# Kernel optimization log

Hardware: AMD Instinct MI355X
Metric: run time of the kernel (lower is better)

The kernel has to match this reference:

```python
import jax, jax.numpy as jnp
import numpy as np

B, N, P, K = 128, 256, 256, 4  # batches, obs points, pred points, nfunc


def setup_inputs() -> dict:
    key = jax.random.key(0)
    k1, k2, k3, k4, k5 = jax.random.split(key, 5)
    # squared distances: symmetric obs-obs block with zero diagonal + obs-pred block
    d_oo = jax.random.uniform(k1, (B, N, N), dtype=jnp.float32) * 25.0
    d_oo = 0.5 * (d_oo + jnp.swapaxes(d_oo, -1, -2))
    d_oo = d_oo * (1.0 - jnp.eye(N, dtype=jnp.float32))
    d_op = jax.random.uniform(k2, (B, N, P), dtype=jnp.float32) * 25.0
    C = jnp.concatenate([d_oo, d_op], axis=-1)  # (B, N, N+P)
    val = jax.random.normal(k3, (B, N, K), dtype=jnp.float32)
    bad = jax.random.randint(k4, (B, N), 0, 10) == 0
    rm = jax.random.normal(k5, (K, 1), dtype=jnp.float32) * 0.1  # MyKF.rm param
    eps_param = -1.5 * jnp.ones((K,), dtype=jnp.float32)          # DistOA.eps param
    return {"C": C, "val": val, "rm": rm, "eps_param": eps_param, "bad": bad}


def _forward(C, val, rm, eps_param, bad):
    n = C.shape[-2]
    # MyKF: x = d2 * sigmoid(rm)/rmax^2 (rmax=1); kernel (1+x)exp(-x)  -> (K,B,n,n+p)
    rmk = jax.nn.sigmoid(rm)[..., None, None]            # (K,1,1,1)
    x = rmk * C[None]
    Cf = (1.0 + x) * jnp.exp(-x)                          # (K,B,n,n+p)
    b = Cf[..., n:]                                       # (K,B,n,p)
    Cm = Cf[..., :n]                                      # (K,B,n,n)
    # implicit: add sigmoid(eps) on the diagonal
    eps = jax.nn.sigmoid(eps_param)[:, None, None, None]  # (K,1,1,1)
    Cm = Cm + eps * jnp.eye(n, dtype=C.dtype)
    # NaN/bad masking: zero bad rows of b; zero xor(bad_i, bad_j) entries of C
    good = (~bad).astype(C.dtype)                         # (B,n)
    b = b * good[None, :, :, None]
    keep = (~(bad[:, :, None] ^ bad[:, None, :])).astype(C.dtype)  # (B,n,n)
    Cm = Cm * keep[None]
    # batched solve + clamp-based reweighting (edging=False)
    d = jnp.linalg.solve(Cm, b)                           # (K,B,n,p)
    wg = jnp.clip((jnp.abs(d).sum(-2, keepdims=True) - 1.0) * 2.0, 0.0, 1.0)
    d1 = b / Cm.sum(-1, keepdims=True)
    r = d * (1.0 - wg) + d1 * (wg / jnp.clip(d1.sum(-2, keepdims=True), 1.0, None))
    # neddvalgrad=False -> val detached before nan_to_num
    val0 = jnp.nan_to_num(jax.lax.stop_gradient(val))     # (B,n,K)
    return jnp.einsum('kbjp,bjk->bpk', r, val0)           # (B,p,K)


def reference(C, val, rm, eps_param, bad):
    return _forward(C, val, rm, eps_param, bad)
```

## Files before the change

### kernel.cpp

```cpp
#include <hip/hip_runtime.h>
#include <cstddef>

#define NN 256
#define PP 256
#define BB 128
#define KK 4
#define NSYS 512
#define PW 32
#define NPAN (NN/PW)

__device__ __forceinline__ float sigmoidf_(float x){ return 1.0f/(1.0f+expf(-x)); }

__global__ __launch_bounds__(256) void build_kernel(
    const float* __restrict__ C, const float* __restrict__ rm,
    const float* __restrict__ epsp, const int* __restrict__ bad,
    float* __restrict__ A, float* __restrict__ rowsum, int s0)
{
  const int si = blockIdx.x;
  const int ls = si >> 8;
  const int i  = si & 255;
  const int s  = s0 + ls;
  const int k  = s >> 7;
  const int b  = s & 127;
  const int j  = threadIdx.x;

  const float sk = sigmoidf_(rm[k]);
  const float ek = sigmoidf_(epsp[k]);
  const bool bad_i = bad[b*NN + i] != 0;
  const bool bad_j = bad[b*NN + j] != 0;

  float c  = C[((size_t)b*NN + i)*(NN+PP) + j];
  float x  = sk * c;
  float cf = (1.0f + x) * expf(-x);
  if (i == j) cf += ek;
  float keep = (bad_i == bad_j) ? 1.0f : 0.0f;
  float a = cf * keep;
  A[((size_t)ls*NN + i)*NN + j] = a;

  __shared__ float red[256];
  red[j] = a; __syncthreads();
  #pragma unroll
  for (int off = 128; off > 0; off >>= 1){
    if (j < off) red[j] += red[j + off];
    __syncthreads();
  }
  if (j == 0) rowsum[ls*NN + i] = red[0];
}

__global__ __launch_bounds__(512, 4) void lu_kernel(
    float* __restrict__ Aall, int* __restrict__ permAll)
{
  __shared__ float panel[NN][PW+1];
  __shared__ float linv[PW][PW+1];
  __shared__ float uinv[PW][PW+1];
  __shared__ float urow[PW][NN-PW];
  __shared__ float redv[2][8];
  __shared__ int   redi[2][8];
  __shared__ int   pivseq[NN];
  __shared__ int   actlist[NN];
  __shared__ unsigned char pickedsh[NN];
  __shared__ int   nact;

  const int ls = blockIdx.x;
  float* __restrict__ A = Aall + (size_t)ls*NN*NN;
  const int t = threadIdx.x;
  const int lane = t & 63, wid = t >> 6;
  bool picked = false;
  if (t < NN) pickedsh[t] = 0;

  for (int I = 0; I < NPAN; ++I){
    const int col0 = I*PW;
    const int W = NN - col0 - PW;
    if (t == 0) nact = 0;
    __syncthreads();

    for (int e = t; e < NN*PW; e += 512){
      int r = e >> 5, c = e & 31;
      panel[r][c] = A[(size_t)r*NN + col0 + c];
    }
    __syncthreads();

    {
      float v = -1.0f; int vi = 0;
      if (t < NN && !picked){ v = fabsf(panel[t][0]); vi = t; }
      #pragma unroll
      for (int off = 32; off > 0; off >>= 1){
        float ov = __shfl_down(v, off); int oi = __shfl_down(vi, off);
        if (ov > v){ v = ov; vi = oi; }
      }
      if (lane == 0){ redv[0][wid] = v; redi[0][wid] = vi; }
    }
    __syncthreads();

    for (int c = 0; c < PW; ++c){
      const int par = c & 1;
      float bv = redv[par][0]; int p = redi[par][0];
      #pragma unroll
      for (int w = 1; w < 8; ++w)
        if (redv[par][w] > bv){ bv = redv[par][w]; p = redi[par][w]; }
      if (t == p){ picked = true; pickedsh[t] = 1; pivseq[col0+c] = t; }

      float nv = -1.0f; int ni = t;
      if (t < NN && !picked){
        const float rdia = 1.0f / panel[p][c];
        float m = panel[t][c] * rdia;
        panel[t][c] = m;
        float nxt = -1.0f;
        #pragma unroll
        for (int j = 0; j < PW; ++j){
          if (j > c){
            float u = panel[t][j] - m * panel[p][j];
            panel[t][j] = u;
            if (j == c+1) nxt = fabsf(u);
          }
        }
        nv = nxt;
      }
      #pragma unroll
      for (int off = 32; off > 0; off >>= 1){
        float ov = __shfl_down(nv, off); int oi = __shfl_down(ni, off);
        if (ov > nv){ nv = ov; ni = oi; }
      }
      if (lane == 0){ redv[par^1][wid] = nv; redi[par^1][wid] = ni; }
      __syncthreads();
    }

    if (t >= 256){
      const int jj = t - 256;
      if (jj < W){
        const int j = col0 + PW + jj;
        float u[PW];
        #pragma unroll
        for (int c = 0; c < PW; ++c) u[c] = A[(size_t)pivseq[col0+c]*NN + j];
        #pragma unroll
        for (int c = 0; c < PW; ++c){
          const int pc = pivseq[col0+c];
          float sv = u[c];
          #pragma unroll
          for (int k2 = 0; k2 < PW; ++k2)
            if (k2 < c) sv -= panel[pc][k2] * u[k2];
          u[c] = sv;
          urow[c][jj] = sv;
          A[(size_t)pc*NN + j] = sv;
        }
      }
    } else if (t < PW){
      const int cth = t;
      for (int r = cth; r < PW; ++r){
        float sv = (r == cth) ? 1.0f : 0.0f;
        const int pr = pivseq[col0+r];
        for (int k2 = cth; k2 < r; ++k2) sv -= panel[pr][k2] * linv[k2][cth];
        linv[r][cth] = sv;
      }
    } else if (t >= 64 && t < 64+PW){
      const int cth = t - 64;
      for (int r = cth; r >= 0; --r){
        float sv = (r == cth) ? 1.0f : 0.0f;
        const int pr = pivseq[col0+r];
        for (int k2 = r+1; k2 <= cth; ++k2) sv -= panel[pr][k2] * uinv[k2][cth];
        uinv[r][cth] = sv / panel[pr][r];
      }
    } else if (t >= 128 && t < 192){
      #pragma unroll
      for (int q = 0; q < 4; ++q){
        int r = (t-128)*4 + q;
        if (!pickedsh[r]){ int pos = atomicAdd(&nact, 1); actlist[pos] = r; }
      }
    }
    __syncthreads();

    for (int e = t; e < PW*PW; e += 512){
      int r = e >> 5, c2 = e & 31;
      A[(size_t)pivseq[col0+r]*NN + col0 + c2] = (r > c2) ? linv[r][c2] : uinv[r][c2];
    }
    for (int e = t; e < NN*PW; e += 512){
      int r = e >> 5, c2 = e & 31;
      if (!pickedsh[r]) A[(size_t)r*NN + col0 + c2] = panel[r][c2];
    }

    if (W > 0){
      for (int i0 = wid*2; i0 < W; i0 += 16){
        const int r0 = actlist[i0];
        const int r1 = actlist[i0+1];
        float4* R0 = (float4*)(A + (size_t)r0*NN + col0 + PW);
        float4* R1 = (float4*)(A + (size_t)r1*NN + col0 + PW);
        if (lane*4 < W){
          float4 a0 = R0[lane];
          float4 a1 = R1[lane];
          #pragma unroll
          for (int c = 0; c < PW; ++c){
            float4 u4 = *(const float4*)&urow[c][lane*4];
            float p0 = panel[r0][c], p1 = panel[r1][c];
            a0.x -= p0*u4.x; a0.y -= p0*u4.y; a0.z -= p0*u4.z; a0.w -= p0*u4.w;
            a1.x -= p1*u4.x; a1.y -= p1*u4.y; a1.z -= p1*u4.z; a1.w -= p1*u4.w;
          }
          R0[lane] = a0;
          R1[lane] = a1;
        }
      }
    }
  }
  __syncthreads();
  if (t < NN) permAll[ls*NN + t] = pivseq[t];
}

__global__ __launch_bounds__(512, 2) void solve_epi_kernel(
    const float* __restrict__ Aall, const int* __restrict__ permAll,
    const float* __restrict__ rowsum,
    const float* __restrict__ C, const float* __restrict__ val,
    const int* __restrict__ bad, const float* __restrict__ rm,
    float* __restrict__ out, int s0)
{
  __shared__ float tile[NN][128];
  __shared__ float dblk[PW][PW+1];
  __shared__ __align__(16) float ubuf[4096];
  __shared__ int   perm[NN];

  int ls, c0;
  {
    const int g = blockIdx.x;
    if ((gridDim.x & 15) == 0){
      const int xcd = g & 7, idx = g >> 3;
      ls = xcd + 8*(idx >> 1);
      c0 = (idx & 1) * 128;
    } else {
      ls = g >> 1;
      c0 = (g & 1) * 128;
    }
  }
  const int s  = s0 + ls;
  const int k  = s >> 7, b = s & 127;
  const float* __restrict__ A = Aall + (size_t)ls*NN*NN;
  const float* __restrict__ rs = rowsum + ls*NN;
  const int t = threadIdx.x;
  const int lane = t & 63, wid = t >> 6;
  const int lane2 = lane + 64;
  const float sk = sigmoidf_(rm[k]);
  const int slr = t >> 3;
  const int sq4 = (t & 7) << 2;

  if (t < NN) perm[t] = permAll[ls*NN + t];
  __syncthreads();

  for (int e = t; e < NN*128; e += 512){
    int i = e >> 7, c = e & 127;
    int pi = perm[i];
    float cb = C[((size_t)b*NN + pi)*(NN+PP) + NN + c0 + c];
    float xb = sk * cb;
    float bf = (1.0f + xb) * expf(-xb);
    if (bad[b*NN + pi]) bf = 0.0f;
    tile[i][c] = bf;
  }
  __syncthreads();

  for (int J = 0; J < NPAN; ++J){
    const int j0 = J*PW;
    for (int e = t; e < PW*PW; e += 512){
      int r = e >> 5, c = e & 31;
      dblk[r][c] = A[(size_t)perm[j0+r]*NN + j0 + c];
    }
    __syncthreads();
    const int r0 = wid*4;
    float ya0 = tile[j0+r0+0][lane],  yb0 = tile[j0+r0+0][lane2];
    float ya1 = tile[j0+r0+1][lane],  yb1 = tile[j0+r0+1][lane2];
    float ya2 = tile[j0+r0+2][lane],  yb2 = tile[j0+r0+2][lane2];
    float ya3 = tile[j0+r0+3][lane],  yb3 = tile[j0+r0+3][lane2];
    for (int kk = 0; kk < r0; ++kk){
      float xa = tile[j0+kk][lane], xb = tile[j0+kk][lane2];
      float d0 = dblk[r0+0][kk], d1 = dblk[r0+1][kk], d2 = dblk[r0+2][kk], d3 = dblk[r0+3][kk];
      ya0 += d0*xa; yb0 += d0*xb;
      ya1 += d1*xa; yb1 += d1*xb;
      ya2 += d2*xa; yb2 += d2*xb;
      ya3 += d3*xa; yb3 += d3*xb;
    }
    {
      float xa0 = tile[j0+r0][lane],  xa1 = tile[j0+r0+1][lane],  xa2 = tile[j0+r0+2][lane];
      float xb0 = tile[j0+r0][lane2], xb1 = tile[j0+r0+1][lane2], xb2 = tile[j0+r0+2][lane2];
      float e10 = dblk[r0+1][r0];
      float e20 = dblk[r0+2][r0], e21 = dblk[r0+2][r0+1];
      float e30 = dblk[r0+3][r0], e31 = dblk[r0+3][r0+1], e32 = dblk[r0+3][r0+2];
      ya1 += e10*xa0;                         yb1 += e10*xb0;
      ya2 += e20*xa0 + e21*xa1;               yb2 += e20*xb0 + e21*xb1;
      ya3 += e30*xa0 + e31*xa1 + e32*xa2;     yb3 += e30*xb0 + e31*xb1 + e32*xb2;
    }
    __syncthreads();
    tile[j0+r0+0][lane]=ya0; tile[j0+r0+0][lane2]=yb0;
    tile[j0+r0+1][lane]=ya1; tile[j0+r0+1][lane2]=yb1;
    tile[j0+r0+2][lane]=ya2; tile[j0+r0+2][lane2]=yb2;
    tile[j0+r0+3][lane]=ya3; tile[j0+r0+3][lane2]=yb3;
    __syncthreads();
    const int nbelow = NN - j0 - PW;
    if (nbelow > 0){
      float xa[PW], xb[PW];
      #pragma unroll
      for (int kk = 0; kk < PW; ++kk){ xa[kk] = tile[j0+kk][lane]; xb[kk] = tile[j0+kk][lane2]; }
      for (int cb2 = 0; cb2 < nbelow; cb2 += 64){
        const int rows_c = (nbelow - cb2 < 64) ? (nbelow - cb2) : 64;
        if (t < rows_c*8)
          *(float4*)&ubuf[(slr<<5) + sq4] =
            *(const float4*)(A + (size_t)perm[j0+PW+cb2+slr]*NN + j0 + sq4);
        __syncthreads();
        const int rpw = rows_c >> 3;
        for (int p2 = 0; p2 < rpw; p2 += 2){
          const int lr0 = wid*rpw + p2;
          const int ia = j0 + PW + cb2 + lr0, ib = ia + 1;
          const float* __restrict__ S0 = &ubuf[lr0<<5];
          const float* __restrict__ S1 = &ubuf[(lr0+1)<<5];
          float a0a = tile[ia][lane], a0b = tile[ia][lane2];
          float a1a = tile[ib][lane], a1b = tile[ib][lane2];
          #pragma unroll
          for (int q = 0; q < 8; ++q){
            float4 a4 = *(const float4*)(S0 + (q<<2));
            float4 b4 = *(const float4*)(S1 + (q<<2));
            a0a -= a4.x*xa[q*4+0] + a4.y*xa[q*4+1] + a4.z*xa[q*4+2] + a4.w*xa[q*4+3];
            a0b -= a4.x*xb[q*4+0] + a4.y*xb[q*4+1] + a4.z*xb[q*4+2] + a4.w*xb[q*4+3];
            a1a -= b4.x*xa[q*4+0] + b4.y*xa[q*4+1] + b4.z*xa[q*4+2] + b4.w*xa[q*4+3];
            a1b -= b4.x*xb[q*4+0] + b4.y*xb[q*4+1] + b4.z*xb[q*4+2] + b4.w*xb[q*4+3];
          }
          tile[ia][lane] = a0a; tile[ia][lane2] = a0b;
          tile[ib][lane] = a1a; tile[ib][lane2] = a1b;
        }
        __syncthreads();
      }
    }
  }

  for (int J = NPAN-1; J >= 0; --J){
    const int j0 = J*PW;
    for (int e = t; e < PW*PW; e += 512){
      int r = e >> 5, c = e & 31;
      dblk[r][c] = A[(size_t)perm[j0+r]*NN + j0 + c];
    }
    __syncthreads();
    const int r0 = wid*4;
    float ya0=0.f, ya1=0.f, ya2=0.f, ya3=0.f;
    float yb0=0.f, yb1=0.f, yb2=0.f, yb3=0.f;
    for (int kk = r0+4; kk < PW; ++kk){
      float xa = tile[j0+kk][lane], xb = tile[j0+kk][lane2];
      float d0 = dblk[r0+0][kk], d1 = dblk[r0+1][kk], d2 = dblk[r0+2][kk], d3 = dblk[r0+3][kk];
      ya0 += d0*xa; yb0 += d0*xb;
      ya1 += d1*xa; yb1 += d1*xb;
      ya2 += d2*xa; yb2 += d2*xb;
      ya3 += d3*xa; yb3 += d3*xb;
    }
    {
      float xa0 = tile[j0+r0][lane],  xa1 = tile[j0+r0+1][lane];
      float xa2 = tile[j0+r0+2][lane], xa3 = tile[j0+r0+3][lane];
      float xb0 = tile[j0+r0][lane2],  xb1 = tile[j0+r0+1][lane2];
      float xb2 = tile[j0+r0+2][lane2], xb3 = tile[j0+r0+3][lane2];
      float e00=dblk[r0][r0], e01=dblk[r0][r0+1], e02=dblk[r0][r0+2], e03=dblk[r0][r0+3];
      float e11=dblk[r0+1][r0+1], e12=dblk[r0+1][r0+2], e13=dblk[r0+1][r0+3];
      float e22=dblk[r0+2][r0+2], e23=dblk[r0+2][r0+3];
      float e33=dblk[r0+3][r0+3];
      ya0 += e00*xa0 + e01*xa1 + e02*xa2 + e03*xa3;  yb0 += e00*xb0 + e01*xb1 + e02*xb2 + e03*xb3;
      ya1 += e11*xa1 + e12*xa2 + e13*xa3;            yb1 += e11*xb1 + e12*xb2 + e13*xb3;
      ya2 += e22*xa2 + e23*xa3;                      yb2 += e22*xb2 + e23*xb3;
      ya3 += e33*xa3;                                yb3 += e33*xb3;
    }
    __syncthreads();
    tile[j0+r0+0][lane]=ya0; tile[j0+r0+0][lane2]=yb0;
    tile[j0+r0+1][lane]=ya1; tile[j0+r0+1][lane2]=yb1;
    tile[j0+r0+2][lane]=ya2; tile[j0+r0+2][lane2]=yb2;
    tile[j0+r0+3][lane]=ya3; tile[j0+r0+3][lane2]=yb3;
    __syncthreads();
    if (j0 > 0){
      float xa[PW], xb[PW];
      #pragma unroll
      for (int kk = 0; kk < PW; ++kk){ xa[kk] = tile[j0+kk][lane]; xb[kk] = tile[j0+kk][lane2]; }
      for (int cb2 = 0; cb2 < j0; cb2 += 64){
        const int rows_c = (j0 - cb2 < 64) ? (j0 - cb2) : 64;
        if (t < rows_c*8)
          *(float4*)&ubuf[(slr<<5) + sq4] =
            *(const float4*)(A + (size_t)perm[cb2+slr]*NN + j0 + sq4);
        __syncthreads();
        const int rpw = rows_c >> 3;
        for (int p2 = 0; p2 < rpw; p2 += 2){
          const int lr0 = wid*rpw + p2;
          const int ia = cb2 + lr0, ib = ia + 1;
          const float* __restrict__ S0 = &ubuf[lr0<<5];
          const float* __restrict__ S1 = &ubuf[(lr0+1)<<5];
          float a0a = tile[ia][lane], a0b = tile[ia][lane2];
          float a1a = tile[ib][lane], a1b = tile[ib][lane2];
          #pragma unroll
          for (int q = 0; q < 8; ++q){
            float4 a4 = *(const float4*)(S0 + (q<<2));
            float4 b4 = *(const float4*)(S1 + (q<<2));
            a0a -= a4.x*xa[q*4+0] + a4.y*xa[q*4+1] + a4.z*xa[q*4+2] + a4.w*xa[q*4+3];
            a0b -= a4.x*xb[q*4+0] + a4.y*xb[q*4+1] + a4.z*xb[q*4+2] + a4.w*xb[q*4+3];
            a1a -= b4.x*xa[q*4+0] + b4.y*xa[q*4+1] + b4.z*xa[q*4+2] + b4.w*xa[q*4+3];
            a1b -= b4.x*xb[q*4+0] + b4.y*xb[q*4+1] + b4.z*xb[q*4+2] + b4.w*xb[q*4+3];
          }
          tile[ia][lane] = a0a; tile[ia][lane2] = a0b;
          tile[ib][lane] = a1a; tile[ib][lane2] = a1b;
        }
        __syncthreads();
      }
    }
  }

  {
    float sdva=0.f, sabsa=0.f, s1va=0.f, s1a=0.f;
    float sdvb=0.f, sabsb=0.f, s1vb=0.f, s1b=0.f;
    const int pa = c0 + lane, pb = c0 + lane2;
    for (int j = wid*32; j < wid*32 + 32; ++j){
      float v = val[(b*NN + j)*KK + k];
      if (v != v) v = 0.0f;
      const float rsj = rs[j];
      const bool bj = bad[b*NN + j] != 0;
      float da = tile[j][lane];
      float cba = C[((size_t)b*NN + j)*(NN+PP) + NN + pa];
      float xba = sk*cba;
      float boa = (1.0f+xba)*expf(-xba);
      if (bj) boa = 0.0f;
      float d1a = boa / rsj;
      sdva += da*v; sabsa += fabsf(da); s1va += d1a*v; s1a += d1a;
      float db = tile[j][lane2];
      float cbb = C[((size_t)b*NN + j)*(NN+PP) + NN + pb];
      float xbb = sk*cbb;
      float bob = (1.0f+xbb)*expf(-xbb);
      if (bj) bob = 0.0f;
      float d1b = bob / rsj;
      sdvb += db*v; sabsb += fabsf(db); s1vb += d1b*v; s1b += d1b;
    }
    __syncthreads();
    ubuf[(0*8 + wid)*128 + lane] = sdva;  ubuf[(0*8 + wid)*128 + lane2] = sdvb;
    ubuf[(1*8 + wid)*128 + lane] = sabsa; ubuf[(1*8 + wid)*128 + lane2] = sabsb;
    ubuf[(2*8 + wid)*128 + lane] = s1va;  ubuf[(2*8 + wid)*128 + lane2] = s1vb;
    ubuf[(3*8 + wid)*128 + lane] = s1a;   ubuf[(3*8 + wid)*128 + lane2] = s1b;
  }
  __syncthreads();
  if (t < 128){
    float sdv=0.f, sabs=0.f, s1v=0.f, s1=0.f;
    #pragma unroll
    for (int w = 0; w < 8; ++w){
      sdv  += ubuf[(0*8 + w)*128 + t];
      sabs += ubuf[(1*8 + w)*128 + t];
      s1v  += ubuf[(2*8 + w)*128 + t];
      s1   += ubuf[(3*8 + w)*128 + t];
    }
    float wg    = fminf(fmaxf((sabs - 1.0f)*2.0f, 0.0f), 1.0f);
    float denom = fmaxf(s1, 1.0f);
    out[((size_t)b*PP + c0 + t)*KK + k] = (1.0f - wg)*sdv + (wg/denom)*s1v;
  }
}

extern "C" void kernel_launch(void* const* d_in, const int* in_sizes, int n_in,
                              void* d_out, int out_size, void* d_ws, size_t ws_size,
                              hipStream_t stream)
{
  (void)in_sizes; (void)n_in; (void)out_size;
  const float* C    = (const float*)d_in[0];
  const float* val  = (const float*)d_in[1];
  const float* rm   = (const float*)d_in[2];
  const float* epsp = (const float*)d_in[3];
  const int*   bad  = (const int*)d_in[4];
  float* out = (float*)d_out;

  const size_t per_sys = (size_t)NN*NN*4 + (size_t)NN*4 + (size_t)NN*4;
  int chunk = (int)(ws_size / per_sys);
  if (chunk < 1)    chunk = 1;
  if (chunk > NSYS) chunk = NSYS;

  float* ws     = (float*)d_ws;
  float* A      = ws;
  float* rowsum = A + (size_t)chunk*NN*NN;
  int*   perm   = (int*)(rowsum + (size_t)chunk*NN);

  for (int s0 = 0; s0 < NSYS; s0 += chunk){
    int cs = (NSYS - s0 < chunk) ? (NSYS - s0) : chunk;
    build_kernel<<<cs*NN, 256, 0, stream>>>(C, rm, epsp, bad, A, rowsum, s0);
    lu_kernel<<<cs, 512, 0, stream>>>(A, perm);
    solve_epi_kernel<<<cs*2, 512, 0, stream>>>(A, perm, rowsum, C, val, bad, rm, out, s0);
  }
}
```

Baseline: 1.529 ms.

## Split solve kernel into four 64-column blocks of 256 threads per system

The triangular-solve/epilogue kernel now assigns 64 right-hand-side columns per block with 256 threads, launching four blocks per system instead of two 512-thread blocks with 128 columns. This halves shared memory per block so more blocks can reside per CU and spreads work over more blocks. In exchange, each block reloads the same LU panels from global/L2 memory, doubling that traffic, and the panel update now processes one row per thread group per pass.

```diff
diff --git a/kernel.cpp b/kernel.cpp
--- a/kernel.cpp
+++ b/kernel.cpp
@@ -204,28 +204,28 @@
   if (t < NN) permAll[ls*NN + t] = pivseq[t];
 }
 
-__global__ __launch_bounds__(512, 2) void solve_epi_kernel(
+__global__ __launch_bounds__(256, 2) void solve_epi_kernel(
     const float* __restrict__ Aall, const int* __restrict__ permAll,
     const float* __restrict__ rowsum,
     const float* __restrict__ C, const float* __restrict__ val,
     const int* __restrict__ bad, const float* __restrict__ rm,
     float* __restrict__ out, int s0)
 {
-  __shared__ float tile[NN][128];
+  __shared__ float tile[NN][64];
   __shared__ float dblk[PW][PW+1];
-  __shared__ __align__(16) float ubuf[4096];
+  __shared__ __align__(16) float ubuf[2048];
   __shared__ int   perm[NN];
 
   int ls, c0;
   {
     const int g = blockIdx.x;
-    if ((gridDim.x & 15) == 0){
+    if ((gridDim.x & 31) == 0){
       const int xcd = g & 7, idx = g >> 3;
-      ls = xcd + 8*(idx >> 1);
-      c0 = (idx & 1) * 128;
+      ls = xcd + 8*(idx >> 2);
+      c0 = (idx & 3) * 64;
     } else {
-      ls = g >> 1;
-      c0 = (g & 1) * 128;
+      ls = g >> 2;
+      c0 = (g & 2 ? 128 : 0) + (g & 1)*64;
     }
   }
   const int s  = s0 + ls;
@@ -233,20 +233,19 @@
   const float* __restrict__ A = Aall + (size_t)ls*NN*NN;
   const float* __restrict__ rs = rowsum + ls*NN;
   const int t = threadIdx.x;
-  const int lane = t & 63, wid = t >> 6;
-  const int lane2 = lane + 64;
+  const int ca = t & 31;
+  const int cb = ca + 32;
+  const int rg = t >> 5;
   const float sk = sigmoidf_(rm[k]);
-  const int slr = t >> 3;
-  const int sq4 = (t & 7) << 2;
 
   if (t < NN) perm[t] = permAll[ls*NN + t];
   __syncthreads();
 
-  for (int e = t; e < NN*128; e += 512){
-    int i = e >> 7, c = e & 127;
+  for (int e = t; e < NN*64; e += 256){
+    int i = e >> 6, c = e & 63;
     int pi = perm[i];
-    float cb = C[((size_t)b*NN + pi)*(NN+PP) + NN + c0 + c];
-    float xb = sk * cb;
+    float cbv = C[((size_t)b*NN + pi)*(NN+PP) + NN + c0 + c];
+    float xb = sk * cbv;
     float bf = (1.0f + xb) * expf(-xb);
     if (bad[b*NN + pi]) bf = 0.0f;
     tile[i][c] = bf;
@@ -255,18 +254,18 @@
 
   for (int J = 0; J < NPAN; ++J){
     const int j0 = J*PW;
-    for (int e = t; e < PW*PW; e += 512){
+    for (int e = t; e < PW*PW; e += 256){
       int r = e >> 5, c = e & 31;
       dblk[r][c] = A[(size_t)perm[j0+r]*NN + j0 + c];
     }
     __syncthreads();
-    const int r0 = wid*4;
-    float ya0 = tile[j0+r0+0][lane],  yb0 = tile[j0+r0+0][lane2];
-    float ya1 = tile[j0+r0+1][lane],  yb1 = tile[j0+r0+1][lane2];
-    float ya2 = tile[j0+r0+2][lane],  yb2 = tile[j0+r0+2][lane2];
-    float ya3 = tile[j0+r0+3][lane],  yb3 = tile[j0+r0+3][lane2];
+    const int r0 = rg*4;
+    float ya0 = tile[j0+r0+0][ca],  yb0 = tile[j0+r0+0][cb];
+    float ya1 = tile[j0+r0+1][ca],  yb1 = tile[j0+r0+1][cb];
+    float ya2 = tile[j0+r0+2][ca],  yb2 = tile[j0+r0+2][cb];
+    float ya3 = tile[j0+r0+3][ca],  yb3 = tile[j0+r0+3][cb];
     for (int kk = 0; kk < r0; ++kk){
-      float xa = tile[j0+kk][lane], xb = tile[j0+kk][lane2];
+      float xa = tile[j0+kk][ca], xb = tile[j0+kk][cb];
       float d0 = dblk[r0+0][kk], d1 = dblk[r0+1][kk], d2 = dblk[r0+2][kk], d3 = dblk[r0+3][kk];
       ya0 += d0*xa; yb0 += d0*xb;
       ya1 += d1*xa; yb1 += d1*xb;
@@ -274,8 +273,8 @@
       ya3 += d3*xa; yb3 += d3*xb;
     }
     {
-      float xa0 = tile[j0+r0][lane],  xa1 = tile[j0+r0+1][lane],  xa2 = tile[j0+r0+2][lane];
-      float xb0 = tile[j0+r0][lane2], xb1 = tile[j0+r0+1][lane2], xb2 = tile[j0+r0+2][lane2];
+      float xa0 = tile[j0+r0][ca],  xa1 = tile[j0+r0+1][ca],  xa2 = tile[j0+r0+2][ca];
+      float xb0 = tile[j0+r0][cb],  xb1 = tile[j0+r0+1][cb],  xb2 = tile[j0+r0+2][cb];
       float e10 = dblk[r0+1][r0];
       float e20 = dblk[r0+2][r0], e21 = dblk[r0+2][r0+1];
       float e30 = dblk[r0+3][r0], e31 = dblk[r0+3][r0+1], e32 = dblk[r0+3][r0+2];
@@ -284,41 +283,38 @@
       ya3 += e30*xa0 + e31*xa1 + e32*xa2;     yb3 += e30*xb0 + e31*xb1 + e32*xb2;
     }
     __syncthreads();
-    tile[j0+r0+0][lane]=ya0; tile[j0+r0+0][lane2]=yb0;
-    tile[j0+r0+1][lane]=ya1; tile[j0+r0+1][lane2]=yb1;
-    tile[j0+r0+2][lane]=ya2; tile[j0+r0+2][lane2]=yb2;
-    tile[j0+r0+3][lane]=ya3; tile[j0+r0+3][lane2]=yb3;
+    tile[j0+r0+0][ca]=ya0; tile[j0+r0+0][cb]=yb0;
+    tile[j0+r0+1][ca]=ya1; tile[j0+r0+1][cb]=yb1;
+    tile[j0+r0+2][ca]=ya2; tile[j0+r0+2][cb]=yb2;
+    tile[j0+r0+3][ca]=ya3; tile[j0+r0+3][cb]=yb3;
     __syncthreads();
     const int nbelow = NN - j0 - PW;
     if (nbelow > 0){
       float xa[PW], xb[PW];
       #pragma unroll
-      for (int kk = 0; kk < PW; ++kk){ xa[kk] = tile[j0+kk][lane]; xb[kk] = tile[j0+kk][lane2]; }
+      for (int kk = 0; kk < PW; ++kk){ xa[kk] = tile[j0+kk][ca]; xb[kk] = tile[j0+kk][cb]; }
       for (int cb2 = 0; cb2 < nbelow; cb2 += 64){
         const int rows_c = (nbelow - cb2 < 64) ? (nbelow - cb2) : 64;
-        if (t < rows_c*8)
-          *(float4*)&ubuf[(slr<<5) + sq4] =
-            *(const float4*)(A + (size_t)perm[j0+PW+cb2+slr]*NN + j0 + sq4);
+        for (int e = t; e < rows_c*8; e += 256){
+          int lr = e >> 3, q = e & 7;
+          *(float4*)&ubuf[(lr<<5) + (q<<2)] =
+            *(const float4*)(A + (size_t)perm[j0+PW+cb2+lr]*NN + j0 + (q<<2));
+        }
         __syncthreads();
-        const int rpw = rows_c >> 3;
-        for (int p2 = 0; p2 < rpw; p2 += 2){
-          const int lr0 = wid*rpw + p2;
-          const int ia = j0 + PW + cb2 + lr0, ib = ia + 1;
-          const float* __restrict__ S0 = &ubuf[lr0<<5];
-          const float* __restrict__ S1 = &ubuf[(lr0+1)<<5];
-          float a0a = tile[ia][lane], a0b = tile[ia][lane2];
-          float a1a = tile[ib][lane], a1b = tile[ib][lane2];
+        for (int p2 = 0; p2 < rows_c; p2 += 8){
+          const int lr = p2 + rg;
+          const int ia = j0 + PW + cb2 + lr;
+          const float* __restrict__ S0 = &ubuf[lr<<5];
+          float acc_a = tile[ia][ca];
+          float acc_b = tile[ia][cb];
           #pragma unroll
           for (int q = 0; q < 8; ++q){
             float4 a4 = *(const float4*)(S0 + (q<<2));
-            float4 b4 = *(const float4*)(S1 + (q<<2));
-            a0a -= a4.x*xa[q*4+0] + a4.y*xa[q*4+1] + a4.z*xa[q*4+2] + a4.w*xa[q*4+3];
-            a0b -= a4.x*xb[q*4+0] + a4.y*xb[q*4+1] + a4.z*xb[q*4+2] + a4.w*xb[q*4+3];
-            a1a -= b4.x*xa[q*4+0] + b4.y*xa[q*4+1] + b4.z*xa[q*4+2] + b4.w*xa[q*4+3];
-            a1b -= b4.x*xb[q*4+0] + b4.y*xb[q*4+1] + b4.z*xb[q*4+2] + b4.w*xb[q*4+3];
+            acc_a -= a4.x*xa[q*4+0] + a4.y*xa[q*4+1] + a4.z*xa[q*4+2] + a4.w*xa[q*4+3];
+            acc_b -= a4.x*xb[q*4+0] + a4.y*xb[q*4+1] + a4.z*xb[q*4+2] + a4.w*xb[q*4+3];
           }
-          tile[ia][lane] = a0a; tile[ia][lane2] = a0b;
-          tile[ib][lane] = a1a; tile[ib][lane2] = a1b;
+          tile[ia][ca] = acc_a;
+          tile[ia][cb] = acc_b;
         }
         __syncthreads();
       }
@@ -327,16 +323,16 @@
 
   for (int J = NPAN-1; J >= 0; --J){
     const int j0 = J*PW;
-    for (int e = t; e < PW*PW; e += 512){
+    for (int e = t; e < PW*PW; e += 256){
       int r = e >> 5, c = e & 31;
       dblk[r][c] = A[(size_t)perm[j0+r]*NN + j0 + c];
     }
     __syncthreads();
-    const int r0 = wid*4;
+    const int r0 = rg*4;
     float ya0=0.f, ya1=0.f, ya2=0.f, ya3=0.f;
     float yb0=0.f, yb1=0.f, yb2=0.f, yb3=0.f;
     for (int kk = r0+4; kk < PW; ++kk){
-      float xa = tile[j0+kk][lane], xb = tile[j0+kk][lane2];
+      float xa = tile[j0+kk][ca], xb = tile[j0+kk][cb];
       float d0 = dblk[r0+0][kk], d1 = dblk[r0+1][kk], d2 = dblk[r0+2][kk], d3 = dblk[r0+3][kk];
       ya0 += d0*xa; yb0 += d0*xb;
       ya1 += d1*xa; yb1 += d1*xb;
@@ -344,10 +340,10 @@
       ya3 += d3*xa; yb3 += d3*xb;
     }
     {
-      float xa0 = tile[j0+r0][lane],  xa1 = tile[j0+r0+1][lane];
-      float xa2 = tile[j0+r0+2][lane], xa3 = tile[j0+r0+3][lane];
-      float xb0 = tile[j0+r0][lane2],  xb1 = tile[j0+r0+1][lane2];
-      float xb2 = tile[j0+r0+2][lane2], xb3 = tile[j0+r0+3][lane2];
+      float xa0 = tile[j0+r0][ca],  xa1 = tile[j0+r0+1][ca];
+      float xa2 = tile[j0+r0+2][ca], xa3 = tile[j0+r0+3][ca];
+      float xb0 = tile[j0+r0][cb],  xb1 = tile[j0+r0+1][cb];
+      float xb2 = tile[j0+r0+2][cb], xb3 = tile[j0+r0+3][cb];
       float e00=dblk[r0][r0], e01=dblk[r0][r0+1], e02=dblk[r0][r0+2], e03=dblk[r0][r0+3];
       float e11=dblk[r0+1][r0+1], e12=dblk[r0+1][r0+2], e13=dblk[r0+1][r0+3];
       float e22=dblk[r0+2][r0+2], e23=dblk[r0+2][r0+3];
@@ -358,40 +354,37 @@
       ya3 += e33*xa3;                                yb3 += e33*xb3;
     }
     __syncthreads();
-    tile[j0+r0+0][lane]=ya0; tile[j0+r0+0][lane2]=yb0;
-    tile[j0+r0+1][lane]=ya1; tile[j0+r0+1][lane2]=yb1;
-    tile[j0+r0+2][lane]=ya2; tile[j0+r0+2][lane2]=yb2;
-    tile[j0+r0+3][lane]=ya3; tile[j0+r0+3][lane2]=yb3;
+    tile[j0+r0+0][ca]=ya0; tile[j0+r0+0][cb]=yb0;
+    tile[j0+r0+1][ca]=ya1; tile[j0+r0+1][cb]=yb1;
+    tile[j0+r0+2][ca]=ya2; tile[j0+r0+2][cb]=yb2;
+    tile[j0+r0+3][ca]=ya3; tile[j0+r0+3][cb]=yb3;
     __syncthreads();
     if (j0 > 0){
       float xa[PW], xb[PW];
       #pragma unroll
-      for (int kk = 0; kk < PW; ++kk){ xa[kk] = tile[j0+kk][lane]; xb[kk] = tile[j0+kk][lane2]; }
+      for (int kk = 0; kk < PW; ++kk){ xa[kk] = tile[j0+kk][ca]; xb[kk] = tile[j0+kk][cb]; }
       for (int cb2 = 0; cb2 < j0; cb2 += 64){
         const int rows_c = (j0 - cb2 < 64) ? (j0 - cb2) : 64;
-        if (t < rows_c*8)
-          *(float4*)&ubuf[(slr<<5) + sq4] =
-            *(const float4*)(A + (size_t)perm[cb2+slr]*NN + j0 + sq4);
+        for (int e = t; e < rows_c*8; e += 256){
+          int lr = e >> 3, q = e & 7;
+          *(float4*)&ubuf[(lr<<5) + (q<<2)] =
+            *(const float4*)(A + (size_t)perm[cb2+lr]*NN + j0 + (q<<2));
+        }
         __syncthreads();
-        const int rpw = rows_c >> 3;
-        for (int p2 = 0; p2 < rpw; p2 += 2){
-          const int lr0 = wid*rpw + p2;
-          const int ia = cb2 + lr0, ib = ia + 1;
-          const float* __restrict__ S0 = &ubuf[lr0<<5];
-          const float* __restrict__ S1 = &ubuf[(lr0+1)<<5];
-          float a0a = tile[ia][lane], a0b = tile[ia][lane2];
-          float a1a = tile[ib][lane], a1b = tile[ib][lane2];
+        for (int p2 = 0; p2 < rows_c; p2 += 8){
+          const int lr = p2 + rg;
+          const int ia = cb2 + lr;
+          const float* __restrict__ S0 = &ubuf[lr<<5];
+          float acc_a = tile[ia][ca];
+          float acc_b = tile[ia][cb];
           #pragma unroll
           for (int q = 0; q < 8; ++q){
             float4 a4 = *(const float4*)(S0 + (q<<2));
-            float4 b4 = *(const float4*)(S1 + (q<<2));
-            a0a -= a4.x*xa[q*4+0] + a4.y*xa[q*4+1] + a4.z*xa[q*4+2] + a4.w*xa[q*4+3];
-            a0b -= a4.x*xb[q*4+0] + a4.y*xb[q*4+1] + a4.z*xb[q*4+2] + a4.w*xb[q*4+3];
-            a1a -= b4.x*xa[q*4+0] + b4.y*xa[q*4+1] + b4.z*xa[q*4+2] + b4.w*xa[q*4+3];
-            a1b -= b4.x*xb[q*4+0] + b4.y*xb[q*4+1] + b4.z*xb[q*4+2] + b4.w*xb[q*4+3];
+            acc_a -= a4.x*xa[q*4+0] + a4.y*xa[q*4+1] + a4.z*xa[q*4+2] + a4.w*xa[q*4+3];
+            acc_b -= a4.x*xb[q*4+0] + a4.y*xb[q*4+1] + a4.z*xb[q*4+2] + a4.w*xb[q*4+3];
           }
-          tile[ia][lane] = a0a; tile[ia][lane2] = a0b;
-          tile[ib][lane] = a1a; tile[ib][lane2] = a1b;
+          tile[ia][ca] = acc_a;
+          tile[ia][cb] = acc_b;
         }
         __syncthreads();
       }
@@ -401,20 +394,20 @@
   {
     float sdva=0.f, sabsa=0.f, s1va=0.f, s1a=0.f;
     float sdvb=0.f, sabsb=0.f, s1vb=0.f, s1b=0.f;
-    const int pa = c0 + lane, pb = c0 + lane2;
-    for (int j = wid*32; j < wid*32 + 32; ++j){
+    const int pa = c0 + ca, pb = c0 + cb;
+    for (int j = rg*32; j < rg*32 + 32; ++j){
       float v = val[(b*NN + j)*KK + k];
       if (v != v) v = 0.0f;
       const float rsj = rs[j];
       const bool bj = bad[b*NN + j] != 0;
-      float da = tile[j][lane];
+      float da = tile[j][ca];
       float cba = C[((size_t)b*NN + j)*(NN+PP) + NN + pa];
       float xba = sk*cba;
       float boa = (1.0f+xba)*expf(-xba);
       if (bj) boa = 0.0f;
       float d1a = boa / rsj;
       sdva += da*v; sabsa += fabsf(da); s1va += d1a*v; s1a += d1a;
-      float db = tile[j][lane2];
+      float db = tile[j][cb];
       float cbb = C[((size_t)b*NN + j)*(NN+PP) + NN + pb];
       float xbb = sk*cbb;
       float bob = (1.0f+xbb)*expf(-xbb);
@@ -423,20 +416,20 @@
       sdvb += db*v; sabsb += fabsf(db); s1vb += d1b*v; s1b += d1b;
     }
     __syncthreads();
-    ubuf[(0*8 + wid)*128 + lane] = sdva;  ubuf[(0*8 + wid)*128 + lane2] = sdvb;
-    ubuf[(1*8 + wid)*128 + lane] = sabsa; ubuf[(1*8 + wid)*128 + lane2] = sabsb;
-    ubuf[(2*8 + wid)*128 + lane] = s1va;  ubuf[(2*8 + wid)*128 + lane2] = s1vb;
-    ubuf[(3*8 + wid)*128 + lane] = s1a;   ubuf[(3*8 + wid)*128 + lane2] = s1b;
+    ubuf[(0*8 + rg)*64 + ca] = sdva;  ubuf[(0*8 + rg)*64 + cb] = sdvb;
+    ubuf[(1*8 + rg)*64 + ca] = sabsa; ubuf[(1*8 + rg)*64 + cb] = sabsb;
+    ubuf[(2*8 + rg)*64 + ca] = s1va;  ubuf[(2*8 + rg)*64 + cb] = s1vb;
+    ubuf[(3*8 + rg)*64 + ca] = s1a;   ubuf[(3*8 + rg)*64 + cb] = s1b;
   }
   __syncthreads();
-  if (t < 128){
+  if (t < 64){
     float sdv=0.f, sabs=0.f, s1v=0.f, s1=0.f;
     #pragma unroll
     for (int w = 0; w < 8; ++w){
-      sdv  += ubuf[(0*8 + w)*128 + t];
-      sabs += ubuf[(1*8 + w)*128 + t];
-      s1v  += ubuf[(2*8 + w)*128 + t];
-      s1   += ubuf[(3*8 + w)*128 + t];
+      sdv  += ubuf[(0*8 + w)*64 + t];
+      sabs += ubuf[(1*8 + w)*64 + t];
+      s1v  += ubuf[(2*8 + w)*64 + t];
+      s1   += ubuf[(3*8 + w)*64 + t];
     }
     float wg    = fminf(fmaxf((sabs - 1.0f)*2.0f, 0.0f), 1.0f);
     float denom = fmaxf(s1, 1.0f);
@@ -470,6 +463,6 @@
     int cs = (NSYS - s0 < chunk) ? (NSYS - s0) : chunk;
     build_kernel<<<cs*NN, 256, 0, stream>>>(C, rm, epsp, bad, A, rowsum, s0);
     lu_kernel<<<cs, 512, 0, stream>>>(A, perm);
-    solve_epi_kernel<<<cs*2, 512, 0, stream>>>(A, perm, rowsum, C, val, bad, rm, out, s0);
+    solve_epi_kernel<<<cs*4, 256, 0, stream>>>(A, perm, rowsum, C, val, bad, rm, out, s0);
   }
 }
```

Result: faster. 1.414 ms (median of 2 runs) (-7.5%).
